# Kernel optimization log

Hardware: AMD Instinct MI355X
Metric: run time of the kernel (lower is better)

Reference implementation:

```python
import jax, jax.numpy as jnp
import numpy as np

SLOPE = 0.01

def leaky_tanh(x):
    return jnp.tanh(x * (2.0 / 3.0)) * 1.7159 + x * SLOPE

def lstm_cell(x, h, c, w_ih, w_hh, b_ih, b_hh):
    # torch LSTMCell gate order: i, f, g, o
    gates = x @ w_ih.T + b_ih + h @ w_hh.T + b_hh
    i, f, g, o = jnp.split(gates, 4, axis=-1)
    c_new = jax.nn.sigmoid(f) * c + jax.nn.sigmoid(i) * jnp.tanh(g)
    h_new = jax.nn.sigmoid(o) * jnp.tanh(c_new)
    return h_new, c_new

def setup_inputs() -> dict:
    key = jax.random.key(0)
    ks = jax.random.split(key, 16)
    T, B, I, H, O = 512, 64, 128, 2048, 64
    H1, H2 = H // 2, H // 8  # 1024, 256
    F2 = H // 4              # 512
    s = 0.02
    return {
        "inputs": jax.random.normal(ks[0], (T, B, I), dtype=jnp.float32),
        "fc1_w": jax.random.normal(ks[1], (H, I), dtype=jnp.float32) * s,
        "fc1_b": jax.random.normal(ks[2], (H,), dtype=jnp.float32) * s,
        "w_ih1": jax.random.normal(ks[3], (4 * H1, H), dtype=jnp.float32) * s,
        "w_hh1": jax.random.normal(ks[4], (4 * H1, H1), dtype=jnp.float32) * s,
        "b_ih1": jax.random.normal(ks[5], (4 * H1,), dtype=jnp.float32) * s,
        "b_hh1": jax.random.normal(ks[6], (4 * H1,), dtype=jnp.float32) * s,
        "fc2_w": jax.random.normal(ks[7], (F2, H1), dtype=jnp.float32) * s,
        "fc2_b": jax.random.normal(ks[8], (F2,), dtype=jnp.float32) * s,
        "w_ih2": jax.random.normal(ks[9], (4 * H2, F2), dtype=jnp.float32) * s,
        "w_hh2": jax.random.normal(ks[10], (4 * H2, H2), dtype=jnp.float32) * s,
        "b_ih2": jax.random.normal(ks[11], (4 * H2,), dtype=jnp.float32) * s,
        "b_hh2": jax.random.normal(ks[12], (4 * H2,), dtype=jnp.float32) * s,
        "fc3_w": jax.random.normal(ks[13], (O, H2), dtype=jnp.float32) * s,
        "fc3_b": jax.random.normal(ks[14], (O,), dtype=jnp.float32) * s,
    }

def reference(inputs, fc1_w, fc1_b, w_ih1, w_hh1, b_ih1, b_hh1,
              fc2_w, fc2_b, w_ih2, w_hh2, b_ih2, b_hh2, fc3_w, fc3_b):
    T, B, _ = inputs.shape
    H1 = w_hh1.shape[1]
    H2 = w_hh2.shape[1]
    h1 = jnp.zeros((B, H1), dtype=inputs.dtype)
    c1 = jnp.zeros((B, H1), dtype=inputs.dtype)
    h2 = jnp.zeros((B, H2), dtype=inputs.dtype)
    c2 = jnp.zeros((B, H2), dtype=inputs.dtype)

    def step(carry, xt):
        h1, c1, h2, c2 = carry
        x = leaky_tanh(xt @ fc1_w.T + fc1_b)
        h1, c1 = lstm_cell(x, h1, c1, w_ih1, w_hh1, b_ih1, b_hh1)
        x = leaky_tanh(h1 @ fc2_w.T + fc2_b)
        h2, c2 = lstm_cell(x, h2, c2, w_ih2, w_hh2, b_ih2, b_hh2)
        yhat = h2 @ fc3_w.T + fc3_b
        return (h1, c1, h2, c2), yhat

    _, outputs = jax.lax.scan(step, (h1, c1, h2, c2), inputs)
    return outputs  # [T, B, output_size]
```

## Files before the change

### kernel.cpp

```cpp
#include <hip/hip_runtime.h>
#include <hip/hip_bf16.h>

static constexpr int T_  = 512;
static constexpr int B_  = 64;
static constexpr int I_  = 128;
static constexpr int H_  = 2048;
static constexpr int H1_ = 1024;
static constexpr int F2_ = 512;
static constexpr int H2_ = 256;
static constexpr int O_  = 64;
static constexpr int G1N = 4096;
static constexpr int G2N = 1024;
static constexpr int NW  = 176;

typedef __attribute__((ext_vector_type(8))) __bf16 bfx8;
typedef __attribute__((ext_vector_type(4))) __bf16 bfx4;
typedef __attribute__((ext_vector_type(4))) float  fx4;

#define DEV __device__ __forceinline__

DEV fx4 mfma16(bfx8 a, bfx8 b, fx4 c) {
  return __builtin_amdgcn_mfma_f32_16x16x32_bf16(a, b, c, 0, 0, 0);
}
DEV float fast_sig(float x) { return 1.0f / (1.0f + __expf(-x)); }
DEV float fast_tanh(float x) {
  x = fminf(fmaxf(x, -30.0f), 30.0f);
  return 2.0f / (1.0f + __expf(-2.0f * x)) - 1.0f;
}
DEV float leaky_tanh_(float x) { return fast_tanh(x * (2.0f / 3.0f)) * 1.7159f + 0.01f * x; }

DEV void gld16(const void* g, void* l) {
  __builtin_amdgcn_global_load_lds(
      (const __attribute__((address_space(1))) unsigned int*)g,
      (__attribute__((address_space(3))) unsigned int*)l, 16, 0, 0);
}
DEV void gld16c(const void* g, void* l) {
  __builtin_amdgcn_global_load_lds(
      (const __attribute__((address_space(1))) unsigned int*)g,
      (__attribute__((address_space(3))) unsigned int*)l, 16, 0, 17);
}
DEV void spin_ge(int* p, int tgt) {
  while (__hip_atomic_load(p, __ATOMIC_RELAXED, __HIP_MEMORY_SCOPE_AGENT) < tgt)
    __builtin_amdgcn_s_sleep(1);
}
DEV void stc2(unsigned short* p, unsigned short v) {
  __hip_atomic_store(p, v, __ATOMIC_RELAXED, __HIP_MEMORY_SCOPE_AGENT);
}
DEV unsigned long long ldc8(const void* p) {
  return __hip_atomic_load((const unsigned long long*)p, __ATOMIC_RELAXED,
                           __HIP_MEMORY_SCOPE_AGENT);
}
DEV unsigned short bf16bits(float f) {
  __bf16 h = (__bf16)f;
  return __builtin_bit_cast(unsigned short, h);
}
DEV void arrive1(int* p) {
  __hip_atomic_fetch_add(p, 1, __ATOMIC_RELAXED, __HIP_MEMORY_SCOPE_AGENT);
}

struct PP {
  const float *fc1w, *wih1f, *whh1f, *fc2w, *wih2f, *whh2f, *fc3w, *fin;
  const float *bih1, *bhh1, *bih2, *bhh2;
  __bf16 *wb_fc1, *wb_ih1, *W2, *wb_fc2, *wb_ih2, *wb_hh2, *wb_fc3, *in_bf;
  float *bsum1, *bsum2, *c1, *c2;
  __bf16 *h1zero, *h2a;
  int *cnt;
};
__global__ void k_prep(PP q) {
  const int bid = blockIdx.x, tid = threadIdx.x;
  if (bid < 2048) {
    int v = bid * 256 + tid;
    int l = v & 63, kk = (v >> 6) & 31, g = (v >> 11) & 3, ng = v >> 13;
    int row = g * 1024 + ng * 16 + (l & 15);
    int k0  = kk * 32 + (l >> 4) * 8;
    const float* sp = q.whh1f + (size_t)row * 1024 + k0;
    float4 v0 = ((const float4*)sp)[0];
    float4 v1 = ((const float4*)sp)[1];
    bfx8 o = { (__bf16)v0.x, (__bf16)v0.y, (__bf16)v0.z, (__bf16)v0.w,
               (__bf16)v1.x, (__bf16)v1.y, (__bf16)v1.z, (__bf16)v1.w };
    *(bfx8*)(q.W2 + (size_t)v * 8) = o;
    return;
  }
  const int gw = (bid - 2048) * 256 + tid, gs = 512 * 256;
  for (int i = gw; i < 65536; i += gs) q.c1[i] = 0.0f;
  for (int i = gw; i < 16384; i += gs) q.c2[i] = 0.0f;
  for (int i = gw; i < 16384; i += gs) ((unsigned*)q.h1zero)[i] = 0u;
  for (int i = gw; i < 8192;  i += gs) ((unsigned*)q.h2a)[i] = 0u;
  for (int i = gw; i < 4096;  i += gs) q.cnt[i] = 0;
  for (int i = gw; i < 4096; i += gs) q.bsum1[i] = q.bih1[i] + q.bhh1[i];
  for (int i = gw; i < 1024; i += gs) q.bsum2[i] = q.bih2[i] + q.bhh2[i];
  auto cv = [&](const float* s, __bf16* d, int n4) {
    for (int i = gw; i < n4; i += gs) {
      float4 v = ((const float4*)s)[i];
      bfx4 o = { (__bf16)v.x, (__bf16)v.y, (__bf16)v.z, (__bf16)v.w };
      ((bfx4*)d)[i] = o;
    }
  };
  cv(q.fc1w,  q.wb_fc1, (H_ * I_) / 4);
  cv(q.wih1f, q.wb_ih1, (G1N * H_) / 4);
  cv(q.fc2w,  q.wb_fc2, (F2_ * H1_) / 4);
  cv(q.wih2f, q.wb_ih2, (G2N * F2_) / 4);
  cv(q.whh2f, q.wb_hh2, (G2N * H2_) / 4);
  cv(q.fc3w,  q.wb_fc3, (O_ * H2_) / 4);
  cv(q.fin,   q.in_bf,  (T_ * B_ * I_) / 4);
}

DEV void gemm_tile(char* sm, const __bf16* __restrict__ A, const __bf16* __restrict__ W,
                   __bf16* __restrict__ outB, const float* __restrict__ bias,
                   int m0, int n0, int N, int K, int epi, int wt)
{
  char* As = sm;
  char* Ws = sm + 16384;
  const int tid = threadIdx.x, lane = tid & 63, wave = tid >> 6;
  const int wm = wave >> 1, wn = wave & 1;
  const int rr = lane & 15, hi = lane >> 4;
  fx4 acc[4][4] = {};
  for (int k0 = 0; k0 < K; k0 += 64) {
    __syncthreads();
#pragma unroll
    for (int i = 0; i < 4; ++i) {
      int idx = i * 256 + tid;
      int r = idx >> 3, cs = (idx & 7) ^ (r & 7);
      gld16(A + (size_t)(m0 + r) * K + k0 + cs * 8, As + idx * 16);
      gld16(W + (size_t)(n0 + r) * K + k0 + cs * 8, Ws + idx * 16);
    }
    __syncthreads();
#pragma unroll
    for (int kh = 0; kh < 2; ++kh) {
      bfx8 a[4], b[4];
      const int cg = kh * 4 + hi;
#pragma unroll
      for (int mi = 0; mi < 4; ++mi) {
        int ra = wm * 64 + mi * 16 + rr;
        a[mi] = *(const bfx8*)(As + ra * 128 + ((cg ^ (ra & 7)) << 4));
      }
#pragma unroll
      for (int ni = 0; ni < 4; ++ni) {
        int rb = wn * 64 + ni * 16 + rr;
        b[ni] = *(const bfx8*)(Ws + rb * 128 + ((cg ^ (rb & 7)) << 4));
      }
#pragma unroll
      for (int mi = 0; mi < 4; ++mi)
#pragma unroll
        for (int ni = 0; ni < 4; ++ni)
          acc[mi][ni] = mfma16(a[mi], b[ni], acc[mi][ni]);
    }
  }
  const int cr = hi * 4, cc = rr;
#pragma unroll
  for (int mi = 0; mi < 4; ++mi)
#pragma unroll
    for (int ni = 0; ni < 4; ++ni) {
      int col = n0 + wn * 64 + ni * 16 + cc;
#pragma unroll
      for (int r = 0; r < 4; ++r) {
        int row = m0 + wm * 64 + mi * 16 + cr + r;
        float v = acc[mi][ni][r] + bias[col];
        if (epi == 1) v = leaky_tanh_(v);
        if (wt) stc2((unsigned short*)outB + ((size_t)row * N + col), bf16bits(v));
        else    outB[(size_t)row * N + col] = (__bf16)v;
      }
    }
}

__launch_bounds__(256)
__global__ void k_gemm(const __bf16* __restrict__ A, const __bf16* __restrict__ W,
                       __bf16* __restrict__ outB, const float* __restrict__ bias,
                       int M, int N, int K, int epi)
{
  __shared__ __align__(16) char sm[32768];
  (void)M;
  gemm_tile(sm, A, W, outB, bias, blockIdx.y * 128, blockIdx.x * 128, N, K, epi, 0);
}

DEV void stage(char* dst, int rsB, const __bf16* __restrict__ src, size_t sStride,
               int n, int lg) {
  for (int idx = threadIdx.x; idx < n; idx += 256) {
    int r = idx >> lg, c = idx & ((1 << lg) - 1);
    *(bfx8*)(dst + r * rsB + ((c * 16) ^ ((r & 7) << 4))) =
        *(const bfx8*)(src + (size_t)r * sStride + c * 8);
  }
}

DEV void fc3_tile(char* smem, const __bf16* __restrict__ h2s,
                  const __bf16* __restrict__ w3, const float* __restrict__ b3,
                  float* __restrict__ out)
{
  const int tid = threadIdx.x, lane = tid & 63, wv = tid >> 6;
  const int rr = lane & 15, hi = lane >> 4;
  char* As = smem;
  char* Ws = smem + 32768;
  stage(As, 512, h2s, 256, 2048, 5);
  stage(Ws, 512, w3, 256, 2048, 5);
  __syncthreads();
  fx4 acc[4] = {};
#pragma unroll
  for (int ks = 0; ks < 8; ++ks) {
    const int cbB = ks * 64 + hi * 16;
    int rb = wv * 16 + rr;
    bfx8 bfr = *(const bfx8*)(Ws + rb * 512 + (cbB ^ ((rb & 7) << 4)));
#pragma unroll
    for (int m = 0; m < 4; ++m) {
      int ra = m * 16 + rr;
      bfx8 afr = *(const bfx8*)(As + ra * 512 + (cbB ^ ((ra & 7) << 4)));
      acc[m] = mfma16(afr, bfr, acc[m]);
    }
  }
  float bv = b3[wv * 16 + rr];
#pragma unroll
  for (int m = 0; m < 4; ++m)
#pragma unroll
    for (int r = 0; r < 4; ++r)
      out[(m * 16 + hi * 4 + r) * 64 + wv * 16 + rr] = acc[m][r] + bv;
}

struct KP {
  const __bf16 *W2, *whh2b, *wfc3;
  const __bf16 *g1rd;  __bf16 *g1wr;
  const __bf16 *xcrd;  __bf16 *xcwr;
  const __bf16 *infc1;
  const __bf16 *h1rd;  const __bf16 *h1s0;  __bf16 *h1wr;
  __bf16 *x2c; __bf16 *g2;
  const __bf16 *wfc1, *wih1, *wfc2, *wih2;
  const float *bfc1, *bs1, *bfc2, *bs2, *b3;
  float *c1, *c2, *out;
  __bf16 *h2a;
  int *cnt;
  int Tc, t0, j0, fc2_tgt, ih2_tgt, pool_off;
  int do_l1, do_l2, do_fc2, do_ih1, do_fc1, do_fc3;
};

__launch_bounds__(256, 1)
__global__ void k_persist3(KP p)
{
  __shared__ __align__(16) char smem[131072];
  const int tid = threadIdx.x, lane = tid & 63, wv = tid >> 6;
  const int rr = lane & 15, hi = lane >> 4;
  const int bid = blockIdx.x;
  int* cnt = p.cnt;
  const int Tc = p.Tc;

  if (bid < 64) {
    if (!p.do_l1) return;
    const int ng = bid;
    char* As = smem;
    float* Cp = (float*)smem;
    const int col = tid & 15, brow = tid >> 4;

    bfx8 wreg[4][8];
#pragma unroll
    for (int g = 0; g < 4; ++g)
#pragma unroll
      for (int j = 0; j < 8; ++j)
        wreg[g][j] = *(const bfx8*)(p.W2 + (size_t)((ng * 4 + g) * 32 + wv * 8 + j) * 512 + lane * 8);

    float pc[4];
#pragma unroll
    for (int q = 0; q < 4; ++q)
      pc[q] = p.c1[(brow + q * 16) * 1024 + ng * 16 + col];

    for (int s = 0; s < Tc; ++s) {
      float pg[4][4];
#pragma unroll
      for (int q = 0; q < 4; ++q)
#pragma unroll
        for (int g = 0; g < 4; ++g)
          pg[q][g] = (float)p.g1rd[(size_t)(s * 64 + brow + q * 16) * 4096 + g * 1024 + ng * 16 + col];

      if (tid < 4) spin_ge(cnt + tid * 128, 16 * (p.t0 + s));
      __syncthreads();

      const __bf16* h1s = (s == 0) ? p.h1s0 : (p.h1wr + (size_t)s * 65536);
      {
        char* dstb = smem + wv * 32768;
#pragma unroll 8
        for (int i = 0; i < 32; ++i) {
          int d = wv * 2048 + i * 64 + lane;
          int r = d >> 7;
          int sg = (r << 7) | ((d & 127) ^ (r & 7));
          gld16c(h1s + (size_t)sg * 8, dstb + i * 1024);
        }
      }
      __syncthreads();

      fx4 acc[4][4] = {};
#pragma unroll
      for (int j = 0; j < 8; ++j) {
        const int kB = (wv * 8 + j) * 64 + hi * 16;
        bfx8 a[4];
#pragma unroll
        for (int m = 0; m < 4; ++m) {
          int ra = m * 16 + rr;
          a[m] = *(const bfx8*)(As + ra * 2048 + (kB ^ ((ra & 7) << 4)));
        }
#pragma unroll
        for (int g = 0; g < 4; ++g)
#pragma unroll
          for (int m = 0; m < 4; ++m)
            acc[g][m] = mfma16(a[m], wreg[g][j], acc[g][m]);
      }
      __syncthreads();
#pragma unroll
      for (int g = 0; g < 4; ++g)
#pragma unroll
        for (int m = 0; m < 4; ++m) {
          int gc = g * 16 + rr;
          int bx = (m * 16 + hi * 4) ^ ((gc & 15) << 2);
          *(fx4*)(Cp + ((wv * 64 + gc) * 64 + bx)) = acc[g][m];
        }
      __syncthreads();

      __bf16* h1o = p.h1wr + (size_t)(s + 1) * 65536;
#pragma unroll
      for (int q = 0; q < 4; ++q) {
        int b_ = brow + q * 16;
        float gv[4];
#pragma unroll
        for (int g = 0; g < 4; ++g) {
          int gc = g * 16 + col;
          int bx = b_ ^ ((gc & 15) << 2);
          float v = pg[q][g];
#pragma unroll
          for (int w = 0; w < 4; ++w)
            v += Cp[(w * 64 + gc) * 64 + bx];
          gv[g] = v;
        }
        float cn = fast_sig(gv[1]) * pc[q] + fast_sig(gv[0]) * fast_tanh(gv[2]);
        pc[q] = cn;
        float hv = fast_sig(gv[3]) * fast_tanh(cn);
        stc2((unsigned short*)h1o + (b_ * 1024 + ng * 16 + col), bf16bits(hv));
      }
      __syncthreads();
      if (tid == 0) arrive1(cnt + (ng & 3) * 128);
    }
#pragma unroll
    for (int q = 0; q < 4; ++q)
      p.c1[(brow + q * 16) * 1024 + ng * 16 + col] = pc[q];

  } else if (bid < 80) {
    if (!p.do_l2) return;
    const int ng2 = bid - 64;
    const int col = tid & 15, brow = tid >> 4;
    char* Ws2 = smem;
    char* As2 = smem + 32768;
    float (*Gx2)[64][16] = (float (*)[64][16])(smem + 32768);

    for (int idx = tid; idx < 2048; idx += 256) {
      int r = idx >> 5, c = idx & 31;
      int wr = (r >> 4) * 256 + ng2 * 16 + (r & 15);
      *(bfx8*)(Ws2 + r * 512 + ((c * 16) ^ ((r & 7) << 4))) =
          *(const bfx8*)(p.whh2b + (size_t)wr * 256 + c * 8);
    }
    float pc2[4];
#pragma unroll
    for (int q = 0; q < 4; ++q)
      pc2[q] = p.c2[(brow + q * 16) * 256 + ng2 * 16 + col];

    if (tid == 0) spin_ge(cnt + 640, p.ih2_tgt);
    __syncthreads();

    for (int s = 0; s < Tc; ++s) {
      float pg[4][4];
#pragma unroll
      for (int q = 0; q < 4; ++q)
#pragma unroll
        for (int g = 0; g < 4; ++g)
          pg[q][g] = (float)p.g2[(size_t)(s * 64 + brow + q * 16) * 1024 + g * 256 + ng2 * 16 + col];

      if (tid == 0) spin_ge(cnt + 512, 16 * (p.j0 + s));
      __syncthreads();

      const __bf16* h2s = p.h2a + (size_t)(p.j0 + s) * 16384;
      for (int idx = tid; idx < 2048; idx += 256) {
        int r = idx >> 5, c = idx & 31;
        const char* sp = (const char*)(h2s + r * 256 + c * 8);
        unsigned long long lo = ldc8(sp), hi8 = ldc8(sp + 8);
        char* dp = As2 + r * 512 + ((c * 16) ^ ((r & 7) << 4));
        *(unsigned long long*)dp = lo;
        *(unsigned long long*)(dp + 8) = hi8;
      }
      __syncthreads();

      fx4 acc[4] = {};
#pragma unroll
      for (int ks = 0; ks < 8; ++ks) {
        const int cb = ks * 64 + hi * 16;
        int rb = wv * 16 + rr;
        bfx8 bfr = *(const bfx8*)(Ws2 + rb * 512 + (cb ^ ((rb & 7) << 4)));
#pragma unroll
        for (int m = 0; m < 4; ++m) {
          int ra = m * 16 + rr;
          bfx8 afr = *(const bfx8*)(As2 + ra * 512 + (cb ^ ((ra & 7) << 4)));
          acc[m] = mfma16(afr, bfr, acc[m]);
        }
      }
      __syncthreads();
#pragma unroll
      for (int m = 0; m < 4; ++m)
#pragma unroll
        for (int r = 0; r < 4; ++r)
          Gx2[wv][m * 16 + hi * 4 + r][rr] = acc[m][r];
      __syncthreads();

      __bf16* h2o = p.h2a + (size_t)(p.j0 + s + 1) * 16384;
#pragma unroll
      for (int q = 0; q < 4; ++q) {
        int b_ = brow + q * 16;
        float gi = Gx2[0][b_][col] + pg[q][0];
        float gf = Gx2[1][b_][col] + pg[q][1];
        float gg = Gx2[2][b_][col] + pg[q][2];
        float go = Gx2[3][b_][col] + pg[q][3];
        float cn = fast_sig(gf) * pc2[q] + fast_sig(gi) * fast_tanh(gg);
        pc2[q] = cn;
        float hv = fast_sig(go) * fast_tanh(cn);
        stc2((unsigned short*)h2o + (b_ * 256 + ng2 * 16 + col), bf16bits(hv));
      }
      __syncthreads();
      if (tid == 0) arrive1(cnt + 512);
    }
#pragma unroll
    for (int q = 0; q < 4; ++q)
      p.c2[(brow + q * 16) * 256 + ng2 * 16 + col] = pc2[q];

  } else {
    const int wid = bid - 80;
    const int Mt = (Tc * 64) / 128;
    if (p.do_fc2) {
      for (int i = wid; i < Mt * 4; i += NW)
        gemm_tile(smem, p.h1rd + 65536, p.wfc2, p.x2c, p.bfc2,
                  (i >> 2) * 128, (i & 3) * 128, F2_, H1_, 1, 1);
      __syncthreads();
      if (tid == 0) { arrive1(cnt + 576); spin_ge(cnt + 576, p.fc2_tgt); }
      __syncthreads();
      for (int i = wid; i < Mt * 8; i += NW)
        gemm_tile(smem, p.x2c, p.wih2, p.g2, p.bs2,
                  (i >> 3) * 128, (i & 7) * 128, G2N, F2_, 0, 1);
      __syncthreads();
      if (tid == 0) arrive1(cnt + 640);
    }
    if (p.do_ih1) {
      for (int i = wid; i < Mt * 32; i += NW)
        gemm_tile(smem, p.xcrd, p.wih1, p.g1wr, p.bs1,
                  (i >> 5) * 128, (i & 31) * 128, G1N, H_, 0, 0);
    }
    if (p.do_fc1) {
      for (int i = wid; i < Mt * 16; i += NW)
        gemm_tile(smem, p.infc1, p.wfc1, p.xcwr, p.bfc1,
                  (i >> 4) * 128, (i & 15) * 128, H_, I_, 1, 0);
    }
    if (p.do_fc3) {
      for (int t = wid; t < T_; t += NW) {
        if (tid == 0) spin_ge(cnt + 512, 16 * (t + 1));
        __syncthreads();
        fc3_tile(smem, p.h2a + (size_t)(t + 1) * 16384, p.wfc3, p.b3,
                 p.out + (size_t)t * 4096);
        __syncthreads();
      }
    }
  }
}

extern "C" void kernel_launch(void* const* d_in, const int* in_sizes, int n_in,
                              void* d_out, int out_size, void* d_ws, size_t ws_size,
                              hipStream_t stream)
{
  (void)in_sizes; (void)n_in; (void)out_size;
  const float* f_in = (const float*)d_in[0];
  const float* fc1w = (const float*)d_in[1];
  const float* fc1b = (const float*)d_in[2];
  const float* wih1 = (const float*)d_in[3];
  const float* whh1 = (const float*)d_in[4];
  const float* bih1 = (const float*)d_in[5];
  const float* bhh1 = (const float*)d_in[6];
  const float* fc2w = (const float*)d_in[7];
  const float* fc2b = (const float*)d_in[8];
  const float* wih2 = (const float*)d_in[9];
  const float* whh2 = (const float*)d_in[10];
  const float* bih2 = (const float*)d_in[11];
  const float* bhh2 = (const float*)d_in[12];
  const float* fc3w = (const float*)d_in[13];
  const float* fc3b = (const float*)d_in[14];
  float* out = (float*)d_out;

  char* base = (char*)d_ws;
  size_t off = 0;
  auto alloc = [&](size_t bytes) -> char* {
    char* q = base + off;
    off = (off + bytes + 255) & ~(size_t)255;
    return q;
  };
  __bf16* wb_fc1 = (__bf16*)alloc((size_t)H_ * I_ * 2);
  __bf16* wb_ih1 = (__bf16*)alloc((size_t)G1N * H_ * 2);
  __bf16* W2     = (__bf16*)alloc((size_t)G1N * H1_ * 2);
  __bf16* wb_fc2 = (__bf16*)alloc((size_t)F2_ * H1_ * 2);
  __bf16* wb_ih2 = (__bf16*)alloc((size_t)G2N * F2_ * 2);
  __bf16* wb_hh2 = (__bf16*)alloc((size_t)G2N * H2_ * 2);
  __bf16* wb_fc3 = (__bf16*)alloc((size_t)O_ * H2_ * 2);
  __bf16* in_bf  = (__bf16*)alloc((size_t)T_ * B_ * I_ * 2);
  float*  bsum1  = (float*) alloc((size_t)G1N * 4);
  float*  bsum2  = (float*) alloc((size_t)G2N * 4);
  float*  c1     = (float*) alloc((size_t)B_ * H1_ * 4);
  float*  c2     = (float*) alloc((size_t)B_ * H2_ * 4);
  __bf16* h2a    = (__bf16*)alloc((size_t)(T_ + 1) * B_ * H2_ * 2);
  __bf16* h1zero = (__bf16*)alloc((size_t)B_ * H1_ * 2);
  int*    cnt    = (int*)   alloc(16384);
  size_t fixed = off;

  auto perTc = [](size_t Tc) -> size_t {
    size_t Mc = Tc * 64;
    return 2 * Mc * H_ * 2 + 2 * Mc * G1N * 2
         + 2 * (Tc + 1) * (size_t)B_ * H1_ * 2
         + Mc * F2_ * 2 + Mc * G2N * 2 + 10 * 256;
  };
  int Tc = 128;
  while (Tc > 8 && fixed + perTc(Tc) > ws_size) Tc >>= 1;
  const int Mc = Tc * 64;
  __bf16* XcA  = (__bf16*)alloc((size_t)Mc * H_ * 2);
  __bf16* XcB  = (__bf16*)alloc((size_t)Mc * H_ * 2);
  __bf16* G1A  = (__bf16*)alloc((size_t)Mc * G1N * 2);
  __bf16* G1B  = (__bf16*)alloc((size_t)Mc * G1N * 2);
  __bf16* h1rA = (__bf16*)alloc((size_t)(Tc + 1) * B_ * H1_ * 2);
  __bf16* h1rB = (__bf16*)alloc((size_t)(Tc + 1) * B_ * H1_ * 2);
  __bf16* x2c  = (__bf16*)alloc((size_t)Mc * F2_ * 2);
  __bf16* G2cb = (__bf16*)alloc((size_t)Mc * G2N * 2);

  PP q;
  q.fc1w = fc1w; q.wih1f = wih1; q.whh1f = whh1; q.fc2w = fc2w;
  q.wih2f = wih2; q.whh2f = whh2; q.fc3w = fc3w; q.fin = f_in;
  q.bih1 = bih1; q.bhh1 = bhh1; q.bih2 = bih2; q.bhh2 = bhh2;
  q.wb_fc1 = wb_fc1; q.wb_ih1 = wb_ih1; q.W2 = W2; q.wb_fc2 = wb_fc2;
  q.wb_ih2 = wb_ih2; q.wb_hh2 = wb_hh2; q.wb_fc3 = wb_fc3; q.in_bf = in_bf;
  q.bsum1 = bsum1; q.bsum2 = bsum2; q.c1 = c1; q.c2 = c2;
  q.h1zero = h1zero; q.h2a = h2a; q.cnt = cnt;
  k_prep<<<2560, 256, 0, stream>>>(q);

  const int chunks = T_ / Tc;
  k_gemm<<<dim3(H_ / 128, (2 * Mc) / 128), 256, 0, stream>>>(
      in_bf, wb_fc1, XcA, fc1b, 2 * Mc, H_, I_, 1);
  k_gemm<<<dim3(G1N / 128, Mc / 128), 256, 0, stream>>>(
      XcA, wb_ih1, G1A, bsum1, Mc, G1N, H_, 0);

  KP p;
  p.W2 = W2; p.whh2b = wb_hh2; p.wfc3 = wb_fc3;
  p.wfc1 = wb_fc1; p.wih1 = wb_ih1; p.wfc2 = wb_fc2; p.wih2 = wb_ih2;
  p.bfc1 = fc1b; p.bs1 = bsum1; p.bfc2 = fc2b; p.bs2 = bsum2; p.b3 = fc3b;
  p.c1 = c1; p.c2 = c2; p.h2a = h2a; p.cnt = cnt; p.out = out;
  p.x2c = x2c; p.g2 = G2cb; p.Tc = Tc;

  for (int k = 0; k < chunks; ++k) {
    p.g1rd = (k & 1) ? G1B : G1A;
    p.g1wr = (k & 1) ? G1A : G1B;
    p.xcrd = ((k + 1) & 1) ? XcB : XcA;
    p.xcwr = (k & 1) ? XcB : XcA;
    p.infc1 = (k + 2 < chunks) ? (in_bf + (size_t)(k + 2) * Mc * I_) : in_bf;
    p.h1wr = (k & 1) ? h1rB : h1rA;
    p.h1rd = (k & 1) ? h1rA : h1rB;
    p.h1s0 = (k == 0) ? h1zero : (p.h1rd + (size_t)Tc * 65536);
    p.t0 = k * Tc;
    p.j0 = (k - 1) * Tc;
    p.fc2_tgt = NW * k;
    p.ih2_tgt = NW * k;
    p.pool_off = 2816 + k * 16;
    p.do_l1 = 1;
    p.do_l2 = (k >= 1);
    p.do_fc2 = (k >= 1);
    p.do_ih1 = (k + 1 < chunks);
    p.do_fc1 = (k + 2 < chunks);
    p.do_fc3 = 0;
    k_persist3<<<256, 256, 0, stream>>>(p);
  }
  p.h1rd = ((chunks - 1) & 1) ? h1rB : h1rA;
  p.h1wr = (p.h1rd == h1rA) ? h1rB : h1rA;
  p.h1s0 = h1zero;
  p.g1rd = G1A; p.g1wr = G1B; p.xcrd = XcA; p.xcwr = XcB; p.infc1 = in_bf;
  p.t0 = 0;
  p.j0 = (chunks - 1) * Tc;
  p.fc2_tgt = NW * chunks;
  p.ih2_tgt = NW * chunks;
  p.pool_off = 2816 + chunks * 16;
  p.do_l1 = 0; p.do_l2 = 1; p.do_fc2 = 1; p.do_ih1 = 0; p.do_fc1 = 0; p.do_fc3 = 1;
  k_persist3<<<256, 256, 0, stream>>>(p);
}
```

Before: 3.376 ms.

## Fuse first-chunk input-to-hidden GEMM into persistent kernel with per-row-block flags

Removes the separate k_gemm launch that computed the layer-1 input gate preactivations for the first chunk. Worker blocks in the first persistent launch now compute those tiles and signal a per-128-row counter, and the layer-1 recurrence waits on the flag for each pair of timesteps. This lets the recurrence start before the whole G1 block is done, at the cost of extra spin-waits and worker blocks that are busy longer in chunk 0. It also drops the cache-policy bits on the h1 LDS loads and removes the unused pool_off field.

```diff
diff --git a/kernel.cpp b/kernel.cpp
--- a/kernel.cpp
+++ b/kernel.cpp
@@ -33,11 +33,6 @@
   __builtin_amdgcn_global_load_lds(
       (const __attribute__((address_space(1))) unsigned int*)g,
       (__attribute__((address_space(3))) unsigned int*)l, 16, 0, 0);
-}
-DEV void gld16c(const void* g, void* l) {
-  __builtin_amdgcn_global_load_lds(
-      (const __attribute__((address_space(1))) unsigned int*)g,
-      (__attribute__((address_space(3))) unsigned int*)l, 16, 0, 17);
 }
 DEV void spin_ge(int* p, int tgt) {
   while (__hip_atomic_load(p, __ATOMIC_RELAXED, __HIP_MEMORY_SCOPE_AGENT) < tgt)
@@ -220,14 +215,15 @@
   const __bf16 *xcrd;  __bf16 *xcwr;
   const __bf16 *infc1;
   const __bf16 *h1rd;  const __bf16 *h1s0;  __bf16 *h1wr;
+  const __bf16 *xc0;   __bf16 *g10;
   __bf16 *x2c; __bf16 *g2;
   const __bf16 *wfc1, *wih1, *wfc2, *wih2;
   const float *bfc1, *bs1, *bfc2, *bs2, *b3;
   float *c1, *c2, *out;
   __bf16 *h2a;
   int *cnt;
-  int Tc, t0, j0, fc2_tgt, ih2_tgt, pool_off;
-  int do_l1, do_l2, do_fc2, do_ih1, do_fc1, do_fc3;
+  int Tc, t0, j0, fc2_tgt, ih2_tgt;
+  int do_l1, do_l2, do_fc2, do_ih1, do_fc1, do_fc3, ih1c;
 };
 
 __launch_bounds__(256, 1)
@@ -261,14 +257,22 @@
 
     for (int s = 0; s < Tc; ++s) {
       float pg[4][4];
-#pragma unroll
-      for (int q = 0; q < 4; ++q)
-#pragma unroll
-        for (int g = 0; g < 4; ++g)
-          pg[q][g] = (float)p.g1rd[(size_t)(s * 64 + brow + q * 16) * 4096 + g * 1024 + ng * 16 + col];
-
-      if (tid < 4) spin_ge(cnt + tid * 128, 16 * (p.t0 + s));
-      __syncthreads();
+      if (!p.ih1c) {
+#pragma unroll
+        for (int q = 0; q < 4; ++q)
+#pragma unroll
+          for (int g = 0; g < 4; ++g)
+            pg[q][g] = (float)p.g1rd[(size_t)(s * 64 + brow + q * 16) * 4096 + g * 1024 + ng * 16 + col];
+        if (tid < 4) spin_ge(cnt + tid * 128, 16 * (p.t0 + s));
+        __syncthreads();
+      } else {
+        if (tid < 5) {
+          int* ad = (tid < 4) ? (cnt + tid * 128) : (cnt + 1024 + ((s >> 1) << 4));
+          int tg = (tid < 4) ? 16 * (p.t0 + s) : 32;
+          spin_ge(ad, tg);
+        }
+        __syncthreads();
+      }
 
       const __bf16* h1s = (s == 0) ? p.h1s0 : (p.h1wr + (size_t)s * 65536);
       {
@@ -278,8 +282,15 @@
           int d = wv * 2048 + i * 64 + lane;
           int r = d >> 7;
           int sg = (r << 7) | ((d & 127) ^ (r & 7));
-          gld16c(h1s + (size_t)sg * 8, dstb + i * 1024);
+          gld16(h1s + (size_t)sg * 8, dstb + i * 1024);
         }
+      }
+      if (p.ih1c) {
+#pragma unroll
+        for (int q = 0; q < 4; ++q)
+#pragma unroll
+          for (int g = 0; g < 4; ++g)
+            pg[q][g] = (float)p.g1rd[(size_t)(s * 64 + brow + q * 16) * 4096 + g * 1024 + ng * 16 + col];
       }
       __syncthreads();
 
@@ -425,6 +436,14 @@
   } else {
     const int wid = bid - 80;
     const int Mt = (Tc * 64) / 128;
+    if (p.ih1c) {
+      for (int i = wid; i < Mt * 32; i += NW) {
+        gemm_tile(smem, p.xc0, p.wih1, p.g10, p.bs1,
+                  (i >> 5) * 128, (i & 31) * 128, G1N, H_, 0, 1);
+        __syncthreads();
+        if (tid == 0) arrive1(cnt + 1024 + ((i >> 5) << 4));
+      }
+    }
     if (p.do_fc2) {
       for (int i = wid; i < Mt * 4; i += NW)
         gemm_tile(smem, p.h1rd + 65536, p.wfc2, p.x2c, p.bfc2,
@@ -537,8 +556,6 @@
   const int chunks = T_ / Tc;
   k_gemm<<<dim3(H_ / 128, (2 * Mc) / 128), 256, 0, stream>>>(
       in_bf, wb_fc1, XcA, fc1b, 2 * Mc, H_, I_, 1);
-  k_gemm<<<dim3(G1N / 128, Mc / 128), 256, 0, stream>>>(
-      XcA, wb_ih1, G1A, bsum1, Mc, G1N, H_, 0);
 
   KP p;
   p.W2 = W2; p.whh2b = wb_hh2; p.wfc3 = wb_fc3;
@@ -546,6 +563,7 @@
   p.bfc1 = fc1b; p.bs1 = bsum1; p.bfc2 = fc2b; p.bs2 = bsum2; p.b3 = fc3b;
   p.c1 = c1; p.c2 = c2; p.h2a = h2a; p.cnt = cnt; p.out = out;
   p.x2c = x2c; p.g2 = G2cb; p.Tc = Tc;
+  p.xc0 = XcA; p.g10 = G1A;
 
   for (int k = 0; k < chunks; ++k) {
     p.g1rd = (k & 1) ? G1B : G1A;
@@ -560,13 +578,13 @@
     p.j0 = (k - 1) * Tc;
     p.fc2_tgt = NW * k;
     p.ih2_tgt = NW * k;
-    p.pool_off = 2816 + k * 16;
     p.do_l1 = 1;
     p.do_l2 = (k >= 1);
     p.do_fc2 = (k >= 1);
     p.do_ih1 = (k + 1 < chunks);
     p.do_fc1 = (k + 2 < chunks);
     p.do_fc3 = 0;
+    p.ih1c = (k == 0);
     k_persist3<<<256, 256, 0, stream>>>(p);
   }
   p.h1rd = ((chunks - 1) & 1) ? h1rB : h1rA;
@@ -577,7 +595,7 @@
   p.j0 = (chunks - 1) * Tc;
   p.fc2_tgt = NW * chunks;
   p.ih2_tgt = NW * chunks;
-  p.pool_off = 2816 + chunks * 16;
   p.do_l1 = 0; p.do_l2 = 1; p.do_fc2 = 1; p.do_ih1 = 0; p.do_fc1 = 0; p.do_fc3 = 1;
+  p.ih1c = 0;
   k_persist3<<<256, 256, 0, stream>>>(p);
 }
```

After: 3.441 ms. About the same (+1.9%).

## Reset counters per chunk launch and move fc3 to a separate batched kernel

Applied to the files above, without the earlier changes.

The synchronisation counters are now zeroed with a memset before every persistent-kernel launch, so spin targets are relative to the chunk instead of cumulative offsets, and the first step skips its spin. The fc3 output projection is removed from the last persistent launch, where worker blocks spun per timestep, and runs as one batched GEMM kernel over all timesteps after the recurrence. This adds several small memset launches but takes the fc3 work and its per-step spinning out of the critical tail. The h1zero clear is also doubled in size.

```diff
diff --git a/kernel.cpp b/kernel.cpp
--- a/kernel.cpp
+++ b/kernel.cpp
@@ -64,7 +64,6 @@
   __bf16 *wb_fc1, *wb_ih1, *W2, *wb_fc2, *wb_ih2, *wb_hh2, *wb_fc3, *in_bf;
   float *bsum1, *bsum2, *c1, *c2;
   __bf16 *h1zero, *h2a;
-  int *cnt;
 };
 __global__ void k_prep(PP q) {
   const int bid = blockIdx.x, tid = threadIdx.x;
@@ -84,9 +83,8 @@
   const int gw = (bid - 2048) * 256 + tid, gs = 512 * 256;
   for (int i = gw; i < 65536; i += gs) q.c1[i] = 0.0f;
   for (int i = gw; i < 16384; i += gs) q.c2[i] = 0.0f;
-  for (int i = gw; i < 16384; i += gs) ((unsigned*)q.h1zero)[i] = 0u;
+  for (int i = gw; i < 32768; i += gs) ((unsigned*)q.h1zero)[i] = 0u;
   for (int i = gw; i < 8192;  i += gs) ((unsigned*)q.h2a)[i] = 0u;
-  for (int i = gw; i < 4096;  i += gs) q.cnt[i] = 0;
   for (int i = gw; i < 4096; i += gs) q.bsum1[i] = q.bih1[i] + q.bhh1[i];
   for (int i = gw; i < 1024; i += gs) q.bsum2[i] = q.bih2[i] + q.bhh2[i];
   auto cv = [&](const float* s, __bf16* d, int n4) {
@@ -182,52 +180,19 @@
   }
 }
 
-DEV void fc3_tile(char* smem, const __bf16* __restrict__ h2s,
-                  const __bf16* __restrict__ w3, const float* __restrict__ b3,
-                  float* __restrict__ out)
-{
-  const int tid = threadIdx.x, lane = tid & 63, wv = tid >> 6;
-  const int rr = lane & 15, hi = lane >> 4;
-  char* As = smem;
-  char* Ws = smem + 32768;
-  stage(As, 512, h2s, 256, 2048, 5);
-  stage(Ws, 512, w3, 256, 2048, 5);
-  __syncthreads();
-  fx4 acc[4] = {};
-#pragma unroll
-  for (int ks = 0; ks < 8; ++ks) {
-    const int cbB = ks * 64 + hi * 16;
-    int rb = wv * 16 + rr;
-    bfx8 bfr = *(const bfx8*)(Ws + rb * 512 + (cbB ^ ((rb & 7) << 4)));
-#pragma unroll
-    for (int m = 0; m < 4; ++m) {
-      int ra = m * 16 + rr;
-      bfx8 afr = *(const bfx8*)(As + ra * 512 + (cbB ^ ((ra & 7) << 4)));
-      acc[m] = mfma16(afr, bfr, acc[m]);
-    }
-  }
-  float bv = b3[wv * 16 + rr];
-#pragma unroll
-  for (int m = 0; m < 4; ++m)
-#pragma unroll
-    for (int r = 0; r < 4; ++r)
-      out[(m * 16 + hi * 4 + r) * 64 + wv * 16 + rr] = acc[m][r] + bv;
-}
-
 struct KP {
-  const __bf16 *W2, *whh2b, *wfc3;
+  const __bf16 *W2, *whh2b;
   const __bf16 *g1rd;  __bf16 *g1wr;
   const __bf16 *xcrd;  __bf16 *xcwr;
   const __bf16 *infc1;
   const __bf16 *h1rd;  const __bf16 *h1s0;  __bf16 *h1wr;
   __bf16 *x2c; __bf16 *g2;
   const __bf16 *wfc1, *wih1, *wfc2, *wih2;
-  const float *bfc1, *bs1, *bfc2, *bs2, *b3;
-  float *c1, *c2, *out;
+  const float *bfc1, *bs1, *bfc2, *bs2;
+  float *c1, *c2;
   __bf16 *h2a;
   int *cnt;
-  int Tc, t0, j0, fc2_tgt, ih2_tgt, pool_off;
-  int do_l1, do_l2, do_fc2, do_ih1, do_fc1, do_fc3;
+  int Tc, t2base, do_l1, do_l2, do_fc2, do_ih1, do_fc1;
 };
 
 __launch_bounds__(256, 1)
@@ -236,6 +201,7 @@
   __shared__ __align__(16) char smem[131072];
   const int tid = threadIdx.x, lane = tid & 63, wv = tid >> 6;
   const int rr = lane & 15, hi = lane >> 4;
+  const int col = tid & 15, brow = tid >> 4;
   const int bid = blockIdx.x;
   int* cnt = p.cnt;
   const int Tc = p.Tc;
@@ -245,7 +211,6 @@
     const int ng = bid;
     char* As = smem;
     float* Cp = (float*)smem;
-    const int col = tid & 15, brow = tid >> 4;
 
     bfx8 wreg[4][8];
 #pragma unroll
@@ -267,7 +232,7 @@
         for (int g = 0; g < 4; ++g)
           pg[q][g] = (float)p.g1rd[(size_t)(s * 64 + brow + q * 16) * 4096 + g * 1024 + ng * 16 + col];
 
-      if (tid < 4) spin_ge(cnt + tid * 128, 16 * (p.t0 + s));
+      if (s > 0 && tid < 4) spin_ge(cnt + tid * 128, 16 * s);
       __syncthreads();
 
       const __bf16* h1s = (s == 0) ? p.h1s0 : (p.h1wr + (size_t)s * 65536);
@@ -340,7 +305,6 @@
   } else if (bid < 80) {
     if (!p.do_l2) return;
     const int ng2 = bid - 64;
-    const int col = tid & 15, brow = tid >> 4;
     char* Ws2 = smem;
     char* As2 = smem + 32768;
     float (*Gx2)[64][16] = (float (*)[64][16])(smem + 32768);
@@ -356,7 +320,7 @@
     for (int q = 0; q < 4; ++q)
       pc2[q] = p.c2[(brow + q * 16) * 256 + ng2 * 16 + col];
 
-    if (tid == 0) spin_ge(cnt + 640, p.ih2_tgt);
+    if (tid == 0) spin_ge(cnt + 640, NW);
     __syncthreads();
 
     for (int s = 0; s < Tc; ++s) {
@@ -367,10 +331,10 @@
         for (int g = 0; g < 4; ++g)
           pg[q][g] = (float)p.g2[(size_t)(s * 64 + brow + q * 16) * 1024 + g * 256 + ng2 * 16 + col];
 
-      if (tid == 0) spin_ge(cnt + 512, 16 * (p.j0 + s));
-      __syncthreads();
-
-      const __bf16* h2s = p.h2a + (size_t)(p.j0 + s) * 16384;
+      if (s > 0 && tid == 0) spin_ge(cnt + 512, 16 * s);
+      __syncthreads();
+
+      const __bf16* h2s = p.h2a + (size_t)(p.t2base + s) * 16384;
       for (int idx = tid; idx < 2048; idx += 256) {
         int r = idx >> 5, c = idx & 31;
         const char* sp = (const char*)(h2s + r * 256 + c * 8);
@@ -402,7 +366,7 @@
           Gx2[wv][m * 16 + hi * 4 + r][rr] = acc[m][r];
       __syncthreads();
 
-      __bf16* h2o = p.h2a + (size_t)(p.j0 + s + 1) * 16384;
+      __bf16* h2o = p.h2a + (size_t)(p.t2base + s + 1) * 16384;
 #pragma unroll
       for (int q = 0; q < 4; ++q) {
         int b_ = brow + q * 16;
@@ -430,7 +394,7 @@
         gemm_tile(smem, p.h1rd + 65536, p.wfc2, p.x2c, p.bfc2,
                   (i >> 2) * 128, (i & 3) * 128, F2_, H1_, 1, 1);
       __syncthreads();
-      if (tid == 0) { arrive1(cnt + 576); spin_ge(cnt + 576, p.fc2_tgt); }
+      if (tid == 0) { arrive1(cnt + 576); spin_ge(cnt + 576, NW); }
       __syncthreads();
       for (int i = wid; i < Mt * 8; i += NW)
         gemm_tile(smem, p.x2c, p.wih2, p.g2, p.bs2,
@@ -448,16 +412,41 @@
         gemm_tile(smem, p.infc1, p.wfc1, p.xcwr, p.bfc1,
                   (i >> 4) * 128, (i & 15) * 128, H_, I_, 1, 0);
     }
-    if (p.do_fc3) {
-      for (int t = wid; t < T_; t += NW) {
-        if (tid == 0) spin_ge(cnt + 512, 16 * (t + 1));
-        __syncthreads();
-        fc3_tile(smem, p.h2a + (size_t)(t + 1) * 16384, p.wfc3, p.b3,
-                 p.out + (size_t)t * 4096);
-        __syncthreads();
-      }
-    }
   }
+}
+
+__launch_bounds__(256)
+__global__ void k_fc3b(const __bf16* __restrict__ H2mat, const __bf16* __restrict__ w3,
+                       const float* __restrict__ b3, float* __restrict__ out)
+{
+  __shared__ __align__(16) char smem[65536];
+  const int tid = threadIdx.x, lane = tid & 63, wv = tid >> 6;
+  const int rr = lane & 15, hi = lane >> 4;
+  char* As = smem;
+  char* Ws = smem + 32768;
+  const size_t row0 = (size_t)blockIdx.x * 64;
+  stage(As, 512, H2mat + row0 * 256, 256, 2048, 5);
+  stage(Ws, 512, w3, 256, 2048, 5);
+  __syncthreads();
+  fx4 acc[4] = {};
+#pragma unroll
+  for (int ks = 0; ks < 8; ++ks) {
+    const int cbB = ks * 64 + hi * 16;
+    int rb = wv * 16 + rr;
+    bfx8 bfr = *(const bfx8*)(Ws + rb * 512 + (cbB ^ ((rb & 7) << 4)));
+#pragma unroll
+    for (int m = 0; m < 4; ++m) {
+      int ra = m * 16 + rr;
+      bfx8 afr = *(const bfx8*)(As + ra * 512 + (cbB ^ ((ra & 7) << 4)));
+      acc[m] = mfma16(afr, bfr, acc[m]);
+    }
+  }
+  float bv = b3[wv * 16 + rr];
+#pragma unroll
+  for (int m = 0; m < 4; ++m)
+#pragma unroll
+    for (int r = 0; r < 4; ++r)
+      out[(row0 + m * 16 + hi * 4 + r) * 64 + wv * 16 + rr] = acc[m][r] + bv;
 }
 
 extern "C" void kernel_launch(void* const* d_in, const int* in_sizes, int n_in,
@@ -503,14 +492,17 @@
   float*  c2     = (float*) alloc((size_t)B_ * H2_ * 4);
   __bf16* h2a    = (__bf16*)alloc((size_t)(T_ + 1) * B_ * H2_ * 2);
   __bf16* h1zero = (__bf16*)alloc((size_t)B_ * H1_ * 2);
-  int*    cnt    = (int*)   alloc(16384);
+  int*    cnt    = (int*)   alloc(4096);
   size_t fixed = off;
 
   auto perTc = [](size_t Tc) -> size_t {
     size_t Mc = Tc * 64;
-    return 2 * Mc * H_ * 2 + 2 * Mc * G1N * 2
+    return 2 * Mc * H_ * 2
+         + 2 * Mc * G1N * 2
          + 2 * (Tc + 1) * (size_t)B_ * H1_ * 2
-         + Mc * F2_ * 2 + Mc * G2N * 2 + 10 * 256;
+         + Mc * F2_ * 2
+         + Mc * G2N * 2
+         + 10 * 256;
   };
   int Tc = 128;
   while (Tc > 8 && fixed + perTc(Tc) > ws_size) Tc >>= 1;
@@ -531,7 +523,7 @@
   q.wb_fc1 = wb_fc1; q.wb_ih1 = wb_ih1; q.W2 = W2; q.wb_fc2 = wb_fc2;
   q.wb_ih2 = wb_ih2; q.wb_hh2 = wb_hh2; q.wb_fc3 = wb_fc3; q.in_bf = in_bf;
   q.bsum1 = bsum1; q.bsum2 = bsum2; q.c1 = c1; q.c2 = c2;
-  q.h1zero = h1zero; q.h2a = h2a; q.cnt = cnt;
+  q.h1zero = h1zero; q.h2a = h2a;
   k_prep<<<2560, 256, 0, stream>>>(q);
 
   const int chunks = T_ / Tc;
@@ -541,13 +533,14 @@
       XcA, wb_ih1, G1A, bsum1, Mc, G1N, H_, 0);
 
   KP p;
-  p.W2 = W2; p.whh2b = wb_hh2; p.wfc3 = wb_fc3;
+  p.W2 = W2; p.whh2b = wb_hh2;
   p.wfc1 = wb_fc1; p.wih1 = wb_ih1; p.wfc2 = wb_fc2; p.wih2 = wb_ih2;
-  p.bfc1 = fc1b; p.bs1 = bsum1; p.bfc2 = fc2b; p.bs2 = bsum2; p.b3 = fc3b;
-  p.c1 = c1; p.c2 = c2; p.h2a = h2a; p.cnt = cnt; p.out = out;
+  p.bfc1 = fc1b; p.bs1 = bsum1; p.bfc2 = fc2b; p.bs2 = bsum2;
+  p.c1 = c1; p.c2 = c2; p.h2a = h2a; p.cnt = cnt;
   p.x2c = x2c; p.g2 = G2cb; p.Tc = Tc;
 
   for (int k = 0; k < chunks; ++k) {
+    hipMemsetAsync(cnt, 0, 4096, stream);
     p.g1rd = (k & 1) ? G1B : G1A;
     p.g1wr = (k & 1) ? G1A : G1B;
     p.xcrd = ((k + 1) & 1) ? XcB : XcA;
@@ -556,28 +549,21 @@
     p.h1wr = (k & 1) ? h1rB : h1rA;
     p.h1rd = (k & 1) ? h1rA : h1rB;
     p.h1s0 = (k == 0) ? h1zero : (p.h1rd + (size_t)Tc * 65536);
-    p.t0 = k * Tc;
-    p.j0 = (k - 1) * Tc;
-    p.fc2_tgt = NW * k;
-    p.ih2_tgt = NW * k;
-    p.pool_off = 2816 + k * 16;
+    p.t2base = (k - 1) * Tc;
     p.do_l1 = 1;
     p.do_l2 = (k >= 1);
     p.do_fc2 = (k >= 1);
     p.do_ih1 = (k + 1 < chunks);
     p.do_fc1 = (k + 2 < chunks);
-    p.do_fc3 = 0;
     k_persist3<<<256, 256, 0, stream>>>(p);
   }
+  hipMemsetAsync(cnt, 0, 4096, stream);
   p.h1rd = ((chunks - 1) & 1) ? h1rB : h1rA;
   p.h1wr = (p.h1rd == h1rA) ? h1rB : h1rA;
   p.h1s0 = h1zero;
   p.g1rd = G1A; p.g1wr = G1B; p.xcrd = XcA; p.xcwr = XcB; p.infc1 = in_bf;
-  p.t0 = 0;
-  p.j0 = (chunks - 1) * Tc;
-  p.fc2_tgt = NW * chunks;
-  p.ih2_tgt = NW * chunks;
-  p.pool_off = 2816 + chunks * 16;
-  p.do_l1 = 0; p.do_l2 = 1; p.do_fc2 = 1; p.do_ih1 = 0; p.do_fc1 = 0; p.do_fc3 = 1;
+  p.t2base = (chunks - 1) * Tc;
+  p.do_l1 = 0; p.do_l2 = 1; p.do_fc2 = 1; p.do_ih1 = 0; p.do_fc1 = 0;
   k_persist3<<<256, 256, 0, stream>>>(p);
-}
+  k_fc3b<<<(T_ * B_) / 64, 256, 0, stream>>>(h2a + (size_t)B_ * H2_, wb_fc3, fc3b, out);
+}
```

Measured after the change: 3.333 ms, median of 2. Within noise of the previous version (-1.3%).
